# Optimization experiments

Measured on AMD Instinct MI355X. Metric: run time of the kernel, lower is better.

## Reference

```python
import jax, jax.numpy as jnp
import numpy as np

HEAD = 8
LN_EPS = 1e-5


def setup_inputs() -> dict:
    key = jax.random.key(0)
    k1, k2, k3, k4 = jax.random.split(key, 4)
    B, N, C = 1, 4096, 128
    x = jax.random.normal(k1, (B, N, C), dtype=jnp.float32)
    A = jax.random.normal(k2, (B, N, HEAD, 1), dtype=jnp.float32)
    # xavier-ish scaled params
    W_qk = jax.random.normal(k3, (C, 2 * C), dtype=jnp.float32) * (1.0 / np.sqrt(C))
    W_v = jax.random.normal(k4, (1, 1), dtype=jnp.float32)
    ln_g = jnp.ones((C,), dtype=jnp.float32)
    ln_b = jnp.zeros((C,), dtype=jnp.float32)
    return {"x": x, "A": A, "W_qk": W_qk, "W_v": W_v, "ln_g": ln_g, "ln_b": ln_b}


def _layernorm(x, g, b):
    mu = jnp.mean(x, axis=-1, keepdims=True)
    var = jnp.mean(jnp.square(x - mu), axis=-1, keepdims=True)
    return (x - mu) * jax.lax.rsqrt(var + LN_EPS) * g + b


def reference(x, A, W_qk, W_v, ln_g, ln_b):
    B, N, C = x.shape
    hd = C // HEAD
    scale = C ** (-0.5)  # NOTE: full dim, as in original (dim ** -0.5)
    xn = _layernorm(x, ln_g, ln_b)
    qk = (xn @ W_qk).reshape(B, N, 2, HEAD, hd)
    q = jnp.transpose(qk[:, :, 0], (0, 2, 1, 3))  # [B,H,N,hd]
    k = jnp.transpose(qk[:, :, 1], (0, 2, 1, 3))  # [B,H,N,hd]
    v = A * W_v[0, 0]                              # Linear(1,1,bias=False)
    v = jnp.transpose(v, (0, 2, 1, 3))             # [B,H,N,1]
    scores = jnp.einsum("bhnd,bhmd->bhnm", q, k) * scale
    attn = jax.nn.softmax(scores, axis=-1)
    out = jnp.einsum("bhnm,bhmv->bhnv", attn, v)   # [B,H,N,1]
    A_plus = jnp.transpose(out, (0, 2, 1, 3))      # [B,N,H,1]
    return A + A_plus
```

## Files before the change

### kernel.cpp

```cpp
#include <hip/hip_runtime.h>

#define HEADS 8
#define NTOK 4096
#define CH 128
#define KSPLIT 8
#define KCHUNK (NTOK / KSPLIT)
#define ROWS 32
#define LN_EPS 1e-5f

typedef short short8 __attribute__((ext_vector_type(8)));
typedef short short4v __attribute__((ext_vector_type(4)));
typedef float f32x4 __attribute__((ext_vector_type(4)));
typedef float f32x2 __attribute__((ext_vector_type(2)));

__device__ inline unsigned short f2bf(float f) {
    unsigned int u = __float_as_uint(f);
    u = (u + 0x7FFFu + ((u >> 16) & 1u)) >> 16;
    return (unsigned short)u;
}

__device__ inline float fast_exp2(float x) {
#if __has_builtin(__builtin_amdgcn_exp2f)
    return __builtin_amdgcn_exp2f(x);
#else
    float r; asm volatile("v_exp_f32 %0, %1" : "=v"(r) : "v"(x)); return r;
#endif
}

__device__ inline f32x2 fma2(f32x2 a, f32x2 b, f32x2 c) {
#if __has_builtin(__builtin_elementwise_fma)
    return __builtin_elementwise_fma(a, b, c);
#else
    f32x2 r; r.x = fmaf(a.x, b.x, c.x); r.y = fmaf(a.y, b.y, c.y); return r;
#endif
}

__device__ inline f32x4 mfma16(short4v a, short4v b, f32x4 c) {
#if __has_builtin(__builtin_amdgcn_mfma_f32_16x16x16bf16_1k)
    return __builtin_amdgcn_mfma_f32_16x16x16bf16_1k(a, b, c, 0, 0, 0);
#elif __has_builtin(__builtin_amdgcn_mfma_f32_16x16x16_bf16)
    return __builtin_amdgcn_mfma_f32_16x16x16_bf16(a, b, c, 0, 0, 0);
#else
    short8 a8 = {a.x, a.y, a.z, a.w, (short)0, (short)0, (short)0, (short)0};
    short8 b8 = {b.x, b.y, b.z, b.w, (short)0, (short)0, (short)0, (short)0};
    return __builtin_amdgcn_mfma_f32_16x16x32_bf16(a8, b8, c, 0, 0, 0);
#endif
}

#define SC (0.08838834764831845f * 1.4426950408889634f)

__global__ __launch_bounds__(256) void ln_qk_fused(
    const float* __restrict__ x, const float* __restrict__ Wqk,
    const float* __restrict__ g, const float* __restrict__ b,
    const float* __restrict__ A,
    unsigned short* __restrict__ qb, unsigned short* __restrict__ kbuf,
    float* __restrict__ vT)
{
    __shared__ __align__(16) unsigned short xn_s[ROWS][CH];
    const int tid = threadIdx.x;
    const int wave = tid >> 6, lane = tid & 63;
    const int row0 = blockIdx.x * ROWS;
    const int ct = blockIdx.y * 4 + wave;
    const int j = lane & 15, grp = lane >> 4;

    const float sc = (ct < 8) ? SC : 1.0f;
    short8 wf[4];
    #pragma unroll
    for (int ks = 0; ks < 4; ++ks) {
        unsigned int uu0, uu1, uu2, uu3;
        const float* wp = Wqk + (ks * 32 + grp * 8) * 256 + ct * 16 + j;
        uu0 = f2bf(wp[0 * 256] * sc) | ((unsigned)f2bf(wp[1 * 256] * sc) << 16);
        uu1 = f2bf(wp[2 * 256] * sc) | ((unsigned)f2bf(wp[3 * 256] * sc) << 16);
        uu2 = f2bf(wp[4 * 256] * sc) | ((unsigned)f2bf(wp[5 * 256] * sc) << 16);
        uu3 = f2bf(wp[6 * 256] * sc) | ((unsigned)f2bf(wp[7 * 256] * sc) << 16);
        uint4 packed = {uu0, uu1, uu2, uu3};
        wf[ks] = *(short8*)&packed;
    }

    if (blockIdx.y == 0) {
        const int hh = tid >> 5, r = tid & 31;
        vT[hh * NTOK + row0 + r] = A[(size_t)(row0 + r) * HEADS + hh];
    }

    for (int rr = wave; rr < ROWS; rr += 4) {
        const int row = row0 + rr;
        float2 xv = *(const float2*)(x + row * CH + lane * 2);
        float s  = xv.x + xv.y;
        float sq = xv.x * xv.x + xv.y * xv.y;
        #pragma unroll
        for (int off = 32; off >= 1; off >>= 1) {
            s  += __shfl_xor(s, off);
            sq += __shfl_xor(sq, off);
        }
        float mu  = s * (1.0f / CH);
        float var = sq * (1.0f / CH) - mu * mu;
        float rs  = rsqrtf(var + LN_EPS);
        float2 gv = *(const float2*)(g + lane * 2);
        float2 bv = *(const float2*)(b + lane * 2);
        unsigned int lo = f2bf((xv.x - mu) * rs * gv.x + bv.x);
        unsigned int hi = f2bf((xv.y - mu) * rs * gv.y + bv.y);
        const int c = (lane * 2) ^ ((rr & 7) << 3);
        *(unsigned int*)&xn_s[rr][c] = lo | (hi << 16);
    }
    __syncthreads();

    #pragma unroll
    for (int t = 0; t < 2; ++t) {
        short8 af[4];
        #pragma unroll
        for (int ks = 0; ks < 4; ++ks)
            af[ks] = *(const short8*)(&xn_s[t * 16 + j]
                                          [(ks * 32 + grp * 8) ^ ((j & 7) << 3)]);

        f32x4 acc = {0.f, 0.f, 0.f, 0.f};
        #pragma unroll
        for (int ks = 0; ks < 4; ++ks)
            acc = __builtin_amdgcn_mfma_f32_16x16x32_bf16(af[ks], wf[ks], acc, 0, 0, 0);

        unsigned short* dst = (ct < 8)
            ? qb   + ((size_t)ct * NTOK + row0 + t * 16) * 16
            : kbuf + ((size_t)(ct - 8) * NTOK + row0 + t * 16) * 16;
        #pragma unroll
        for (int r = 0; r < 4; ++r)
            dst[(grp * 4 + r) * 16 + j] = f2bf(acc[r]);
    }
}

__global__ __launch_bounds__(256) void attn_kernel(
    const unsigned short* __restrict__ qb, const unsigned short* __restrict__ kbuf,
    const float* __restrict__ vT,
    float* __restrict__ partE, float* __restrict__ partF)
{
    const int tid = threadIdx.x;
    const int wave = tid >> 6, lane = tid & 63;
    const int ksp = blockIdx.y, h = blockIdx.z;
    const int q0 = blockIdx.x * 128 + wave * 32;
    const int m0 = ksp * KCHUNK;
    const int j = lane & 15, grp = lane >> 4;

    short4v qf0 = *(const short4v*)(qb + ((size_t)(h * NTOK + q0 + j) * 16 + grp * 4));
    short4v qf1 = *(const short4v*)(qb + ((size_t)(h * NTOK + q0 + 16 + j) * 16 + grp * 4));

    const unsigned short* kl = kbuf + ((size_t)(h * NTOK + m0 + j) * 16 + grp * 4);
    const float* vl = vT + h * NTOK + m0 + grp * 4;

    f32x2 E0 = {0.f, 0.f}, F0 = {0.f, 0.f};
    f32x2 E1 = {0.f, 0.f}, F1 = {0.f, 0.f};

    short4v kf = *(const short4v*)kl;
    f32x4 vv = *(const f32x4*)vl;

    #pragma unroll 4
    for (int mi = 0; mi < KCHUNK; mi += 16) {
        short4v kn = *(const short4v*)(kl + (size_t)(mi + 16) * 16);
        f32x4 vn = *(const f32x4*)(vl + mi + 16);

        f32x4 z = {0.f, 0.f, 0.f, 0.f};
        f32x4 s0 = mfma16(kf, qf0, z);
        f32x4 s1 = mfma16(kf, qf1, z);

        f32x2 p01, p23, r01, r23;
        p01.x = fast_exp2(s0[0]); p01.y = fast_exp2(s0[1]);
        p23.x = fast_exp2(s0[2]); p23.y = fast_exp2(s0[3]);
        r01.x = fast_exp2(s1[0]); r01.y = fast_exp2(s1[1]);
        r23.x = fast_exp2(s1[2]); r23.y = fast_exp2(s1[3]);

        E0 += p01 + p23;
        F0 = fma2(p01, vv.xy, F0);
        F0 = fma2(p23, vv.zw, F0);
        E1 += r01 + r23;
        F1 = fma2(r01, vv.xy, F1);
        F1 = fma2(r23, vv.zw, F1);

        kf = kn; vv = vn;
    }

    float e0 = E0.x + E0.y, f0 = F0.x + F0.y;
    float e1 = E1.x + E1.y, f1 = F1.x + F1.y;

    #pragma unroll
    for (int off = 16; off < 64; off <<= 1) {
        e0 += __shfl_xor(e0, off);
        f0 += __shfl_xor(f0, off);
        e1 += __shfl_xor(e1, off);
        f1 += __shfl_xor(f1, off);
    }

    if (lane < 16) {
        const int base = (ksp * HEADS + h) * NTOK;
        partE[base + q0 + j]      = e0;
        partF[base + q0 + j]      = f0;
        partE[base + q0 + 16 + j] = e1;
        partF[base + q0 + 16 + j] = f1;
    }
}

__global__ __launch_bounds__(256) void reduce_kernel(
    const float* __restrict__ partE, const float* __restrict__ partF,
    const float* __restrict__ A, const float* __restrict__ Wv,
    float* __restrict__ out)
{
    const int t = blockIdx.x * 256 + threadIdx.x;
    const int n = t >> 3;
    const int h = t & 7;
    float E = 0.f, F = 0.f;
    #pragma unroll
    for (int s = 0; s < KSPLIT; ++s) {
        E += partE[(s * HEADS + h) * NTOK + n];
        F += partF[(s * HEADS + h) * NTOK + n];
    }
    out[t] = A[t] + Wv[0] * F / E;
}

extern "C" void kernel_launch(void* const* d_in, const int* in_sizes, int n_in,
                              void* d_out, int out_size, void* d_ws, size_t ws_size,
                              hipStream_t stream)
{
    const float* x   = (const float*)d_in[0];
    const float* A   = (const float*)d_in[1];
    const float* Wqk = (const float*)d_in[2];
    const float* Wv  = (const float*)d_in[3];
    const float* g   = (const float*)d_in[4];
    const float* b   = (const float*)d_in[5];
    float* out = (float*)d_out;

    unsigned short* qb   = (unsigned short*)d_ws;
    unsigned short* kbuf = qb + (size_t)HEADS * NTOK * 16;
    float* vT    = (float*)(kbuf + (size_t)HEADS * NTOK * 16);
    float* partE = vT + (size_t)HEADS * NTOK;
    float* partF = partE + (size_t)KSPLIT * HEADS * NTOK;

    ln_qk_fused<<<dim3(NTOK / ROWS, 4), dim3(256), 0, stream>>>(
        x, Wqk, g, b, A, qb, kbuf, vT);
    attn_kernel<<<dim3(NTOK / 128, KSPLIT, HEADS), dim3(256), 0, stream>>>(
        qb, kbuf, vT, partE, partF);
    reduce_kernel<<<dim3(NTOK * HEADS / 256), dim3(256), 0, stream>>>(
        partE, partF, A, Wv, out);
}
```

Measured before the change: 39.26 us.

## Use 16x16x32 MFMA with zero-padded Q in attention and shrink LN tile

The attention loop now uses the 16x16x32 bf16 MFMA with short8 operands. Q is zero-padded in the upper lanes so that K=16 still maps correctly, instead of relying on the 16x16x16 variant, which may not exist or may be slower on this target. The loop prefetch wraps to index 0 rather than reading past the chunk, and the 4x unroll pragma is dropped. The LN/QK kernel processes 16 rows per block instead of 32, doubling the grid for more parallelism, and the workspace layout is reordered. Half the MFMA K-work is wasted on zeros.

```diff
diff --git a/kernel.cpp b/kernel.cpp
--- a/kernel.cpp
+++ b/kernel.cpp
@@ -5,11 +5,9 @@
 #define CH 128
 #define KSPLIT 8
 #define KCHUNK (NTOK / KSPLIT)
-#define ROWS 32
 #define LN_EPS 1e-5f
 
 typedef short short8 __attribute__((ext_vector_type(8)));
-typedef short short4v __attribute__((ext_vector_type(4)));
 typedef float f32x4 __attribute__((ext_vector_type(4)));
 typedef float f32x2 __attribute__((ext_vector_type(2)));
 
@@ -35,18 +33,6 @@
 #endif
 }
 
-__device__ inline f32x4 mfma16(short4v a, short4v b, f32x4 c) {
-#if __has_builtin(__builtin_amdgcn_mfma_f32_16x16x16bf16_1k)
-    return __builtin_amdgcn_mfma_f32_16x16x16bf16_1k(a, b, c, 0, 0, 0);
-#elif __has_builtin(__builtin_amdgcn_mfma_f32_16x16x16_bf16)
-    return __builtin_amdgcn_mfma_f32_16x16x16_bf16(a, b, c, 0, 0, 0);
-#else
-    short8 a8 = {a.x, a.y, a.z, a.w, (short)0, (short)0, (short)0, (short)0};
-    short8 b8 = {b.x, b.y, b.z, b.w, (short)0, (short)0, (short)0, (short)0};
-    return __builtin_amdgcn_mfma_f32_16x16x32_bf16(a8, b8, c, 0, 0, 0);
-#endif
-}
-
 #define SC (0.08838834764831845f * 1.4426950408889634f)
 
 __global__ __launch_bounds__(256) void ln_qk_fused(
@@ -56,10 +42,10 @@
     unsigned short* __restrict__ qb, unsigned short* __restrict__ kbuf,
     float* __restrict__ vT)
 {
-    __shared__ __align__(16) unsigned short xn_s[ROWS][CH];
+    __shared__ __align__(16) unsigned short xn_s[16][CH];
     const int tid = threadIdx.x;
     const int wave = tid >> 6, lane = tid & 63;
-    const int row0 = blockIdx.x * ROWS;
+    const int row0 = blockIdx.x * 16;
     const int ct = blockIdx.y * 4 + wave;
     const int j = lane & 15, grp = lane >> 4;
 
@@ -77,12 +63,12 @@
         wf[ks] = *(short8*)&packed;
     }
 
-    if (blockIdx.y == 0) {
-        const int hh = tid >> 5, r = tid & 31;
+    if (blockIdx.y == 0 && tid < 128) {
+        const int hh = tid >> 4, r = tid & 15;
         vT[hh * NTOK + row0 + r] = A[(size_t)(row0 + r) * HEADS + hh];
     }
 
-    for (int rr = wave; rr < ROWS; rr += 4) {
+    for (int rr = wave; rr < 16; rr += 4) {
         const int row = row0 + rr;
         float2 xv = *(const float2*)(x + row * CH + lane * 2);
         float s  = xv.x + xv.y;
@@ -104,26 +90,22 @@
     }
     __syncthreads();
 
-    #pragma unroll
-    for (int t = 0; t < 2; ++t) {
-        short8 af[4];
-        #pragma unroll
-        for (int ks = 0; ks < 4; ++ks)
-            af[ks] = *(const short8*)(&xn_s[t * 16 + j]
-                                          [(ks * 32 + grp * 8) ^ ((j & 7) << 3)]);
-
-        f32x4 acc = {0.f, 0.f, 0.f, 0.f};
-        #pragma unroll
-        for (int ks = 0; ks < 4; ++ks)
-            acc = __builtin_amdgcn_mfma_f32_16x16x32_bf16(af[ks], wf[ks], acc, 0, 0, 0);
-
-        unsigned short* dst = (ct < 8)
-            ? qb   + ((size_t)ct * NTOK + row0 + t * 16) * 16
-            : kbuf + ((size_t)(ct - 8) * NTOK + row0 + t * 16) * 16;
-        #pragma unroll
-        for (int r = 0; r < 4; ++r)
-            dst[(grp * 4 + r) * 16 + j] = f2bf(acc[r]);
-    }
+    short8 af[4];
+    #pragma unroll
+    for (int ks = 0; ks < 4; ++ks)
+        af[ks] = *(const short8*)(&xn_s[j][(ks * 32 + grp * 8) ^ ((j & 7) << 3)]);
+
+    f32x4 acc = {0.f, 0.f, 0.f, 0.f};
+    #pragma unroll
+    for (int ks = 0; ks < 4; ++ks)
+        acc = __builtin_amdgcn_mfma_f32_16x16x32_bf16(af[ks], wf[ks], acc, 0, 0, 0);
+
+    unsigned short* dst = (ct < 8)
+        ? qb   + ((size_t)ct * NTOK + row0) * 16
+        : kbuf + ((size_t)(ct - 8) * NTOK + row0) * 16;
+    #pragma unroll
+    for (int r = 0; r < 4; ++r)
+        dst[(grp * 4 + r) * 16 + j] = f2bf(acc[r]);
 }
 
 __global__ __launch_bounds__(256) void attn_kernel(
@@ -136,28 +118,31 @@
     const int ksp = blockIdx.y, h = blockIdx.z;
     const int q0 = blockIdx.x * 128 + wave * 32;
     const int m0 = ksp * KCHUNK;
-    const int j = lane & 15, grp = lane >> 4;
-
-    short4v qf0 = *(const short4v*)(qb + ((size_t)(h * NTOK + q0 + j) * 16 + grp * 4));
-    short4v qf1 = *(const short4v*)(qb + ((size_t)(h * NTOK + q0 + 16 + j) * 16 + grp * 4));
-
-    const unsigned short* kl = kbuf + ((size_t)(h * NTOK + m0 + j) * 16 + grp * 4);
-    const float* vl = vT + h * NTOK + m0 + grp * 4;
+    const int j = lane & 15;
+    const int grp = lane >> 4;
+    const int kh = grp & 1;
+
+    short8 qf0 = *(const short8*)(qb + ((size_t)(h * NTOK + q0 + j) * 16 + kh * 8));
+    short8 qf1 = *(const short8*)(qb + ((size_t)(h * NTOK + q0 + 16 + j) * 16 + kh * 8));
+    if (lane >= 32) { qf0 = (short8)0; qf1 = (short8)0; }
+
+    const unsigned short* kbase = kbuf + ((size_t)h * NTOK + m0) * 16;
+    const float* vbase = vT + h * NTOK + m0 + grp * 4;
 
     f32x2 E0 = {0.f, 0.f}, F0 = {0.f, 0.f};
     f32x2 E1 = {0.f, 0.f}, F1 = {0.f, 0.f};
 
-    short4v kf = *(const short4v*)kl;
-    f32x4 vv = *(const f32x4*)vl;
-
-    #pragma unroll 4
+    short8 kf = *(const short8*)(kbase + (j * 16 + kh * 8));
+    f32x4 vv = *(const f32x4*)vbase;
+
     for (int mi = 0; mi < KCHUNK; mi += 16) {
-        short4v kn = *(const short4v*)(kl + (size_t)(mi + 16) * 16);
-        f32x4 vn = *(const f32x4*)(vl + mi + 16);
+        const int nx = (mi + 16 < KCHUNK) ? mi + 16 : 0;
+        short8 kn = *(const short8*)(kbase + ((nx + j) * 16 + kh * 8));
+        f32x4 vn = *(const f32x4*)(vbase + nx);
 
         f32x4 z = {0.f, 0.f, 0.f, 0.f};
-        f32x4 s0 = mfma16(kf, qf0, z);
-        f32x4 s1 = mfma16(kf, qf1, z);
+        f32x4 s0 = __builtin_amdgcn_mfma_f32_16x16x32_bf16(kf, qf0, z, 0, 0, 0);
+        f32x4 s1 = __builtin_amdgcn_mfma_f32_16x16x32_bf16(kf, qf1, z, 0, 0, 0);
 
         f32x2 p01, p23, r01, r23;
         p01.x = fast_exp2(s0[0]); p01.y = fast_exp2(s0[1]);
@@ -224,13 +209,13 @@
     const float* b   = (const float*)d_in[5];
     float* out = (float*)d_out;
 
-    unsigned short* qb   = (unsigned short*)d_ws;
+    float* partE = (float*)d_ws;
+    float* partF = partE + KSPLIT * HEADS * NTOK;
+    unsigned short* qb   = (unsigned short*)(partF + KSPLIT * HEADS * NTOK);
     unsigned short* kbuf = qb + (size_t)HEADS * NTOK * 16;
-    float* vT    = (float*)(kbuf + (size_t)HEADS * NTOK * 16);
-    float* partE = vT + (size_t)HEADS * NTOK;
-    float* partF = partE + (size_t)KSPLIT * HEADS * NTOK;
-
-    ln_qk_fused<<<dim3(NTOK / ROWS, 4), dim3(256), 0, stream>>>(
+    float* vT = (float*)(kbuf + (size_t)HEADS * NTOK * 16);
+
+    ln_qk_fused<<<dim3(NTOK / 16, 4), dim3(256), 0, stream>>>(
         x, Wqk, g, b, A, qb, kbuf, vT);
     attn_kernel<<<dim3(NTOK / 128, KSPLIT, HEADS), dim3(256), 0, stream>>>(
         qb, kbuf, vT, partE, partF);
```

New measurement: 39.83 us. About the same (+1.5%).
